# Kernel tuning notes

Hardware: AMD Instinct MI355X
Metric: run time of the kernel (lower is better)

The kernel has to match this reference:

```python
import jax, jax.numpy as jnp
import numpy as np

B, L, E, H = 2, 2048, 1024, 16
D = E // H


def setup_inputs() -> dict:
    key = jax.random.key(0)
    ks = jax.random.split(key, 6)
    s = 1.0 / np.sqrt(E)
    return {
        "X": jax.random.normal(ks[0], (B, L, E), dtype=jnp.float32),
        "ke_bias": jax.random.normal(ks[1], (B * H, L, L), dtype=jnp.float32) * 0.05,
        "in_proj_w": jax.random.normal(ks[2], (3 * E, E), dtype=jnp.float32) * s,
        "in_proj_b": jnp.zeros((3 * E,), dtype=jnp.float32),
        "out_proj_w": jax.random.normal(ks[3], (E, E), dtype=jnp.float32) * s,
        "out_proj_b": jnp.zeros((E,), dtype=jnp.float32),
    }


def reference(X, ke_bias, in_proj_w, in_proj_b, out_proj_w, out_proj_b):
    # Packed QKV projection, matching nn.MultiheadAttention layout.
    qkv = X @ in_proj_w.T + in_proj_b  # [B, L, 3E]
    q, k, v = jnp.split(qkv, 3, axis=-1)
    # [B, L, E] -> [B, H, L, D]
    q = q.reshape(B, L, H, D).transpose(0, 2, 1, 3)
    k = k.reshape(B, L, H, D).transpose(0, 2, 1, 3)
    v = v.reshape(B, L, H, D).transpose(0, 2, 1, 3)
    scale = 1.0 / jnp.sqrt(jnp.asarray(D, dtype=q.dtype))
    scores = jnp.einsum("bhqd,bhkd->bhqk", q * scale, k)
    scores = scores + ke_bias.reshape(B, H, L, L)  # additive knowledge bias
    A = jax.nn.softmax(scores, axis=-1)
    ctx = jnp.einsum("bhqk,bhkd->bhqd", A, v)  # [B, H, L, D]
    ctx = ctx.transpose(0, 2, 1, 3).reshape(B, L, E)
    return ctx @ out_proj_w.T + out_proj_b
```

## Files before the change

### kernel.cpp

```cpp
#include <hip/hip_runtime.h>
#include <stdint.h>

typedef __attribute__((ext_vector_type(4))) float f32x4;
typedef __attribute__((ext_vector_type(8))) short bf16x8;
typedef __attribute__((ext_vector_type(4))) short bf16x4;

#define MFMA(a, b, c) __builtin_amdgcn_mfma_f32_16x16x32_bf16(a, b, c, 0, 0, 0)

__device__ __forceinline__ short f2bf(float f) {
    unsigned u = __builtin_bit_cast(unsigned, f);
    u = (u + 0x7fffu + ((u >> 16) & 1u)) >> 16;
    return (short)u;
}

__device__ __forceinline__ void g2l16(const void* g, void* l) {
    __builtin_amdgcn_global_load_lds(
        (const __attribute__((address_space(1))) unsigned*)g,
        (__attribute__((address_space(3))) unsigned*)l, 16, 0, 0);
}

__global__ void cvt_bf16_kernel(const float* __restrict__ src,
                                short* __restrict__ dst, int n8) {
    int i = blockIdx.x * blockDim.x + threadIdx.x;
    if (i >= n8) return;
    const f32x4* s = (const f32x4*)src;
    f32x4 a = s[2 * i], b = s[2 * i + 1];
    bf16x8 o;
    o[0] = f2bf(a[0]); o[1] = f2bf(a[1]); o[2] = f2bf(a[2]); o[3] = f2bf(a[3]);
    o[4] = f2bf(b[0]); o[5] = f2bf(b[1]); o[6] = f2bf(b[2]); o[7] = f2bf(b[3]);
    ((bf16x8*)dst)[i] = o;
}

__global__ __launch_bounds__(256, 2) void gemm_qkv_kernel(
    const short* __restrict__ A, const short* __restrict__ W,
    const float* __restrict__ bias,
    short* __restrict__ qb, short* __restrict__ kb, short* __restrict__ vtb) {
    __shared__ short As[128 * 32];
    __shared__ short Bs[128 * 32];
    __shared__ short scrS[4][16 * 24];
    const int tid = threadIdx.x;
    const int wave = tid >> 6, lane = tid & 63;
    const int al = lane >> 4, ac = lane & 15;
    const int m0 = blockIdx.x * 128;
    const int n0 = blockIdx.y * 128;
    const int wm = wave & 1, wn = wave >> 1;

    const int crow = tid >> 2, ccol = (tid & 3) * 8;
    const short* Ag0 = A + (m0 + crow) * 1024 + ccol;
    const short* Ag1 = A + (m0 + crow + 64) * 1024 + ccol;
    const short* Wg0 = W + (n0 + crow) * 1024 + ccol;
    const short* Wg1 = W + (n0 + crow + 64) * 1024 + ccol;
    short* lA0 = &As[wave * 512];
    short* lA1 = &As[2048 + wave * 512];
    short* lB0 = &Bs[wave * 512];
    short* lB1 = &Bs[2048 + wave * 512];

    f32x4 acc[4][4];
#pragma unroll
    for (int mi = 0; mi < 4; mi++)
#pragma unroll
        for (int ni = 0; ni < 4; ni++) acc[mi][ni] = (f32x4){0.f, 0.f, 0.f, 0.f};

    for (int k0 = 0; k0 < 1024; k0 += 32) {
        __syncthreads();
        g2l16(Ag0 + k0, lA0);
        g2l16(Ag1 + k0, lA1);
        g2l16(Wg0 + k0, lB0);
        g2l16(Wg1 + k0, lB1);
        __syncthreads();
        bf16x8 af[4], bfr[4];
#pragma unroll
        for (int i = 0; i < 4; i++) {
            af[i] = *(const bf16x8*)&As[(wm * 64 + i * 16 + ac) * 32 + al * 8];
            bfr[i] = *(const bf16x8*)&Bs[(wn * 64 + i * 16 + ac) * 32 + al * 8];
        }
#pragma unroll
        for (int mi = 0; mi < 4; mi++)
#pragma unroll
            for (int ni = 0; ni < 4; ni++)
                acc[mi][ni] = MFMA(af[mi], bfr[ni], acc[mi][ni]);
    }

    const int n0w = n0 + wn * 64;
    const int which = n0w >> 10;
    short* scr = scrS[wave];
    const int lr = lane >> 2;
    const int lq = lane & 3;
    const int bglob = m0 >> 11;

#pragma unroll
    for (int mi = 0; mi < 4; mi++) {
#pragma unroll
        for (int ni = 0; ni < 4; ni++) {
            const int col0 = n0w + ni * 16;
            const float bvc = bias[col0 + ac];
            if (which == 2) {
                bf16x4 pk;
#pragma unroll
                for (int r = 0; r < 4; r++) pk[r] = f2bf(acc[mi][ni][r] + bvc);
                *(bf16x4*)&scr[ac * 24 + al * 4] = pk;
                bf16x4 v4 = *(const bf16x4*)&scr[lr * 24 + lq * 4];
                const int colv = col0 + lr;
                const int e = colv & 1023;
                const int h = e >> 6, d = e & 63;
                const int row0 = m0 + wm * 64 + mi * 16 + lq * 4;
                const int l0 = row0 & 2047;
                *(bf16x4*)&vtb[(((bglob * 16 + h) * 64 + d) * 2048) + l0] = v4;
            } else {
                const float sc = (which == 0) ? 0.125f : 1.0f;
#pragma unroll
                for (int r = 0; r < 4; r++)
                    scr[(al * 4 + r) * 24 + ac] = f2bf((acc[mi][ni][r] + bvc) * sc);
                bf16x4 v4 = *(const bf16x4*)&scr[lr * 24 + lq * 4];
                const int col = col0 + lq * 4;
                const int e = col & 1023;
                const int h = e >> 6, d0 = e & 63;
                const int row = m0 + wm * 64 + mi * 16 + lr;
                const int l = row & 2047;
                short* dst = (which == 0) ? qb : kb;
                *(bf16x4*)&dst[(((bglob * 16 + h) * 2048 + l) * 64) + d0] = v4;
            }
        }
    }
}

__global__ __launch_bounds__(256, 4) void attn_kernel(
    const short* __restrict__ Qb, const short* __restrict__ Kb,
    const short* __restrict__ Vtb, const float* __restrict__ bias,
    short* __restrict__ Ctx) {
    __shared__ short Qs[64 * 72];
    __shared__ short Ks[64 * 72];
    __shared__ short Vs[64 * 72];
    __shared__ short Ps[4][16 * 72];
    const int tid = threadIdx.x;
    const int wave = tid >> 6, lane = tid & 63;
    const int al = lane >> 4, ac = lane & 15;
    const int q0 = blockIdx.x * 64;
    const int bh = blockIdx.y;
    const long long kvbase = (long long)bh * (2048 * 64);

    const int sr = tid >> 3, sg = (tid & 7) * 8;

    *(bf16x8*)&Qs[sr * 72 + sg] = *(const bf16x8*)&Qb[kvbase + (q0 + sr) * 64 + sg];
    *(bf16x8*)&Qs[(sr + 32) * 72 + sg] =
        *(const bf16x8*)&Qb[kvbase + (q0 + sr + 32) * 64 + sg];
    __syncthreads();
    const bf16x8 qf0 = *(const bf16x8*)&Qs[(wave * 16 + ac) * 72 + al * 8];
    const bf16x8 qf1 = *(const bf16x8*)&Qs[(wave * 16 + ac) * 72 + al * 8 + 32];

    float m_i[4], l_i[4];
    f32x4 o[4];
#pragma unroll
    for (int r = 0; r < 4; r++) { m_i[r] = -1e30f; l_i[r] = 0.f; }
#pragma unroll
    for (int ni = 0; ni < 4; ni++) o[ni] = (f32x4){0.f, 0.f, 0.f, 0.f};

    const float L2E = 1.44269504088896340736f;
    const float* bp =
        bias + ((long long)bh * 2048 + q0 + wave * 16 + al * 4) * 2048 + ac;

    bf16x8 kr0 = *(const bf16x8*)&Kb[kvbase + sr * 64 + sg];
    bf16x8 kr1 = *(const bf16x8*)&Kb[kvbase + (sr + 32) * 64 + sg];
    bf16x8 vr0 = *(const bf16x8*)&Vtb[kvbase + sr * 2048 + sg];
    bf16x8 vr1 = *(const bf16x8*)&Vtb[kvbase + (sr + 32) * 2048 + sg];
    float bc[16];
#pragma unroll
    for (int ni = 0; ni < 4; ni++)
#pragma unroll
        for (int r = 0; r < 4; r++) bc[ni * 4 + r] = bp[r * 2048 + ni * 16];

#pragma unroll 2
    for (int kbk = 0; kbk < 32; ++kbk) {
        __syncthreads();
        *(bf16x8*)&Ks[sr * 72 + sg] = kr0;
        *(bf16x8*)&Ks[(sr + 32) * 72 + sg] = kr1;
        *(bf16x8*)&Vs[sr * 72 + sg] = vr0;
        *(bf16x8*)&Vs[(sr + 32) * 72 + sg] = vr1;
        __syncthreads();

        const int k1 = (kbk + 1) * 64;
        if (kbk < 31) {
            kr0 = *(const bf16x8*)&Kb[kvbase + (k1 + sr) * 64 + sg];
            kr1 = *(const bf16x8*)&Kb[kvbase + (k1 + sr + 32) * 64 + sg];
            vr0 = *(const bf16x8*)&Vtb[kvbase + sr * 2048 + k1 + sg];
            vr1 = *(const bf16x8*)&Vtb[kvbase + (sr + 32) * 2048 + k1 + sg];
        }

        f32x4 s[4];
#pragma unroll
        for (int ni = 0; ni < 4; ni++) {
            const bf16x8 kf0 = *(const bf16x8*)&Ks[(ni * 16 + ac) * 72 + al * 8];
            const bf16x8 kf1 =
                *(const bf16x8*)&Ks[(ni * 16 + ac) * 72 + al * 8 + 32];
            s[ni] = MFMA(qf0, kf0, ((f32x4){0.f, 0.f, 0.f, 0.f}));
            s[ni] = MFMA(qf1, kf1, s[ni]);
        }
        float mloc[4] = {-1e30f, -1e30f, -1e30f, -1e30f};
#pragma unroll
        for (int ni = 0; ni < 4; ni++)
#pragma unroll
            for (int r = 0; r < 4; r++) {
                float v = (s[ni][r] + bc[ni * 4 + r]) * L2E;
                s[ni][r] = v;
                mloc[r] = fmaxf(mloc[r], v);
            }
#pragma unroll
        for (int r = 0; r < 4; r++) {
#pragma unroll
            for (int off = 1; off < 16; off <<= 1)
                mloc[r] = fmaxf(mloc[r], __shfl_xor(mloc[r], off));
            const float mn = fmaxf(m_i[r], mloc[r]);
            const float a = __builtin_exp2f(m_i[r] - mn);
            m_i[r] = mn;
            l_i[r] *= a;
#pragma unroll
            for (int ni = 0; ni < 4; ni++) o[ni][r] *= a;
        }
        float rs[4] = {0.f, 0.f, 0.f, 0.f};
#pragma unroll
        for (int ni = 0; ni < 4; ni++)
#pragma unroll
            for (int r = 0; r < 4; r++) {
                const float p = __builtin_exp2f(s[ni][r] - m_i[r]);
                rs[r] += p;
                Ps[wave][(al * 4 + r) * 72 + ni * 16 + ac] = f2bf(p);
            }
#pragma unroll
        for (int r = 0; r < 4; r++) {
#pragma unroll
            for (int off = 1; off < 16; off <<= 1) rs[r] += __shfl_xor(rs[r], off);
            l_i[r] += rs[r];
        }

        float bn[16];
        if (kbk < 31) {
#pragma unroll
            for (int ni = 0; ni < 4; ni++)
#pragma unroll
                for (int r = 0; r < 4; r++)
                    bn[ni * 4 + r] = bp[r * 2048 + k1 + ni * 16];
        }

        const bf16x8 pf0 = *(const bf16x8*)&Ps[wave][ac * 72 + al * 8];
        const bf16x8 pf1 = *(const bf16x8*)&Ps[wave][ac * 72 + al * 8 + 32];
#pragma unroll
        for (int ni = 0; ni < 4; ni++) {
            const bf16x8 vf0 = *(const bf16x8*)&Vs[(ni * 16 + ac) * 72 + al * 8];
            const bf16x8 vf1 =
                *(const bf16x8*)&Vs[(ni * 16 + ac) * 72 + al * 8 + 32];
            o[ni] = MFMA(pf0, vf0, o[ni]);
            o[ni] = MFMA(pf1, vf1, o[ni]);
        }
#pragma unroll
        for (int i = 0; i < 16; i++) bc[i] = bn[i];
    }

    const int b = bh >> 4, h = bh & 15;
#pragma unroll
    for (int r = 0; r < 4; r++) {
        const float inv = 1.f / l_i[r];
        const int qrow = q0 + wave * 16 + al * 4 + r;
#pragma unroll
        for (int ni = 0; ni < 4; ni++) {
            const int d = ni * 16 + ac;
            Ctx[((long long)(b * 2048 + qrow)) * 1024 + h * 64 + d] =
                f2bf(o[ni][r] * inv);
        }
    }
}

__global__ __launch_bounds__(256, 2) void gemm_out_kernel(
    const short* __restrict__ A, const short* __restrict__ W,
    const float* __restrict__ bias, float* __restrict__ out) {
    __shared__ short As[128 * 32];
    __shared__ short Bs[128 * 32];
    __shared__ float scrF[4][16 * 28];
    const int tid = threadIdx.x;
    const int wave = tid >> 6, lane = tid & 63;
    const int al = lane >> 4, ac = lane & 15;
    const int m0 = blockIdx.x * 128;
    const int n0 = blockIdx.y * 128;
    const int wm = wave & 1, wn = wave >> 1;

    const int crow = tid >> 2, ccol = (tid & 3) * 8;
    const short* Ag0 = A + (m0 + crow) * 1024 + ccol;
    const short* Ag1 = A + (m0 + crow + 64) * 1024 + ccol;
    const short* Wg0 = W + (n0 + crow) * 1024 + ccol;
    const short* Wg1 = W + (n0 + crow + 64) * 1024 + ccol;
    short* lA0 = &As[wave * 512];
    short* lA1 = &As[2048 + wave * 512];
    short* lB0 = &Bs[wave * 512];
    short* lB1 = &Bs[2048 + wave * 512];

    f32x4 acc[4][4];
#pragma unroll
    for (int mi = 0; mi < 4; mi++)
#pragma unroll
        for (int ni = 0; ni < 4; ni++) acc[mi][ni] = (f32x4){0.f, 0.f, 0.f, 0.f};

    for (int k0 = 0; k0 < 1024; k0 += 32) {
        __syncthreads();
        g2l16(Ag0 + k0, lA0);
        g2l16(Ag1 + k0, lA1);
        g2l16(Wg0 + k0, lB0);
        g2l16(Wg1 + k0, lB1);
        __syncthreads();
        bf16x8 af[4], bfr[4];
#pragma unroll
        for (int i = 0; i < 4; i++) {
            af[i] = *(const bf16x8*)&As[(wm * 64 + i * 16 + ac) * 32 + al * 8];
            bfr[i] = *(const bf16x8*)&Bs[(wn * 64 + i * 16 + ac) * 32 + al * 8];
        }
#pragma unroll
        for (int mi = 0; mi < 4; mi++)
#pragma unroll
            for (int ni = 0; ni < 4; ni++)
                acc[mi][ni] = MFMA(af[mi], bfr[ni], acc[mi][ni]);
    }

    float* scr = scrF[wave];
    const int lr = lane >> 2, lq = lane & 3;
#pragma unroll
    for (int mi = 0; mi < 4; mi++) {
#pragma unroll
        for (int ni = 0; ni < 4; ni++) {
            const int col0 = n0 + wn * 64 + ni * 16;
            const float bvc = bias[col0 + ac];
#pragma unroll
            for (int r = 0; r < 4; r++)
                scr[(al * 4 + r) * 28 + ac] = acc[mi][ni][r] + bvc;
            f32x4 v4 = *(const f32x4*)&scr[lr * 28 + lq * 4];
            const int row = m0 + wm * 64 + mi * 16 + lr;
            *(f32x4*)&out[row * 1024 + col0 + lq * 4] = v4;
        }
    }
}

extern "C" void kernel_launch(void* const* d_in, const int* in_sizes, int n_in,
                              void* d_out, int out_size, void* d_ws,
                              size_t ws_size, hipStream_t stream) {
    const float* X = (const float*)d_in[0];
    const float* keb = (const float*)d_in[1];
    const float* Wi = (const float*)d_in[2];
    const float* bi = (const float*)d_in[3];
    const float* Wo = (const float*)d_in[4];
    const float* bo = (const float*)d_in[5];
    float* out = (float*)d_out;

    char* ws = (char*)d_ws;
    short* Xb  = (short*)(ws);
    short* Wib = (short*)(ws + 8388608);
    short* Wob = (short*)(ws + 14680064);
    short* Qb  = (short*)(ws + 16777216);
    short* Kb  = (short*)(ws + 25165824);
    short* Vtb = (short*)(ws + 33554432);
    short* Ctx = (short*)(ws + 41943040);

    cvt_bf16_kernel<<<dim3(524288 / 256), 256, 0, stream>>>(X, Xb, 524288);
    cvt_bf16_kernel<<<dim3(393216 / 256), 256, 0, stream>>>(Wi, Wib, 393216);
    cvt_bf16_kernel<<<dim3(131072 / 256), 256, 0, stream>>>(Wo, Wob, 131072);
    gemm_qkv_kernel<<<dim3(32, 24), 256, 0, stream>>>(Xb, Wib, bi, Qb, Kb, Vtb);
    attn_kernel<<<dim3(32, 32), 256, 0, stream>>>(Qb, Kb, Vtb, keb, Ctx);
    gemm_out_kernel<<<dim3(32, 8), 256, 0, stream>>>(Ctx, Wob, bo, out);
}
```

Before: 799.7 us.

## Rewrite attention as single-wave LDS-free kernel with transposed S and lazy rescale

The attention kernel becomes one-wave blocks over 16 query rows. K and V fragments are read straight from global memory into registers, so the LDS staging and block barriers are gone. S is computed transposed so the bias can be loaded as float4 nontemporal vectors, and log2e is folded into the Q scale and a bias FMA. Packed bf16 conversion builds the P fragment in registers, rescaling of the output is skipped unless the max grows by more than 8, and setprio is placed around the MFMAs. The risks are more redundant global/L2 traffic for K and V across blocks and a changed block-to-head mapping.

```diff
diff --git a/kernel.cpp b/kernel.cpp
--- a/kernel.cpp
+++ b/kernel.cpp
@@ -13,11 +13,20 @@
     return (short)u;
 }
 
+__device__ __forceinline__ unsigned cvt_pk_bf16(float lo, float hi) {
+    unsigned r;
+    asm("v_cvt_pk_bf16_f32 %0, %1, %2" : "=v"(r) : "v"(lo), "v"(hi));
+    return r;
+}
+
 __device__ __forceinline__ void g2l16(const void* g, void* l) {
     __builtin_amdgcn_global_load_lds(
         (const __attribute__((address_space(1))) unsigned*)g,
         (__attribute__((address_space(3))) unsigned*)l, 16, 0, 0);
 }
+
+union U8 { bf16x8 v; unsigned u[4]; };
+union V8 { bf16x8 v; bf16x4 h[2]; };
 
 __global__ void cvt_bf16_kernel(const float* __restrict__ src,
                                 short* __restrict__ dst, int n8) {
@@ -107,7 +116,7 @@
                 const int l0 = row0 & 2047;
                 *(bf16x4*)&vtb[(((bglob * 16 + h) * 64 + d) * 2048) + l0] = v4;
             } else {
-                const float sc = (which == 0) ? 0.125f : 1.0f;
+                const float sc = (which == 0) ? 0.18033688f : 1.0f;
 #pragma unroll
                 for (int r = 0; r < 4; r++)
                     scr[(al * 4 + r) * 24 + ac] = f2bf((acc[mi][ni][r] + bvc) * sc);
@@ -124,148 +133,129 @@
     }
 }
 
-__global__ __launch_bounds__(256, 4) void attn_kernel(
+#define ATTN_STEP(K0, BC, BN)                                                 \
+  {                                                                           \
+    const int kp_ = ((K0) + 64 < 2048) ? (K0) + 64 : 1984;                    \
+    f32x4 s_[4];                                                              \
+    __builtin_amdgcn_s_setprio(1);                                            \
+    _Pragma("unroll") for (int ni = 0; ni < 4; ni++) {                        \
+        s_[ni] = MFMA(kf[2 * ni], qf0, ((f32x4){0.f, 0.f, 0.f, 0.f}));        \
+        s_[ni] = MFMA(kf[2 * ni + 1], qf1, s_[ni]);                           \
+    }                                                                         \
+    __builtin_amdgcn_s_setprio(0);                                            \
+             \
+    _Pragma("unroll") for (int ni = 0; ni < 4; ni++) {                        \
+        kf[2 * ni] = *(const bf16x8*)&kpb[(kp_ + ni * 16) * 64];              \
+        kf[2 * ni + 1] = *(const bf16x8*)&kpb[(kp_ + ni * 16) * 64 + 32];     \
+    }                                                                         \
+        \
+    V8 vf_[4][2];                                                             \
+    _Pragma("unroll") for (int nd = 0; nd < 4; nd++)                          \
+        _Pragma("unroll") for (int ss = 0; ss < 2; ss++) {                    \
+            const short* vp_ = vpb + nd * (16 * 2048) + (K0) + 32 * ss;       \
+            vf_[nd][ss].h[0] = *(const bf16x4*)vp_;                           \
+            vf_[nd][ss].h[1] = *(const bf16x4*)(vp_ + 16);                    \
+        }                                                                     \
+         \
+    _Pragma("unroll") for (int ni = 0; ni < 4; ni++)                          \
+        BN[ni] = __builtin_nontemporal_load((const f32x4*)&bp[kp_ + ni * 16]);\
+    float t_[16];                                                             \
+    _Pragma("unroll") for (int ni = 0; ni < 4; ni++)                          \
+        _Pragma("unroll") for (int r = 0; r < 4; r++)                         \
+            t_[ni * 4 + r] = __builtin_fmaf(BC[ni][r], L2E, s_[ni][r]);       \
+    float ma_[8];                                                             \
+    _Pragma("unroll") for (int i = 0; i < 8; i++)                             \
+        ma_[i] = fmaxf(t_[i], t_[8 + i]);                                     \
+    float ml_ = fmaxf(fmaxf(fmaxf(ma_[0], ma_[1]), fmaxf(ma_[2], ma_[3])),    \
+                      fmaxf(fmaxf(ma_[4], ma_[5]), fmaxf(ma_[6], ma_[7])));   \
+    ml_ = fmaxf(ml_, __shfl_xor(ml_, 16));                                    \
+    ml_ = fmaxf(ml_, __shfl_xor(ml_, 32));                                    \
+    if (__any(ml_ > m_i + 8.f)) {                \
+        const float mn_ = fmaxf(m_i, ml_);                                    \
+        const float a_ = __builtin_exp2f(m_i - mn_);                          \
+        m_i = mn_;                                                            \
+        l_i *= a_;                                                            \
+        _Pragma("unroll") for (int r = 0; r < 4; r++) {                       \
+            const float ar_ = __shfl(a_, al20 + r);                           \
+            _Pragma("unroll") for (int nd = 0; nd < 4; nd++)                  \
+                o[nd][r] *= ar_;                                              \
+        }                                                                     \
+    }                                                                         \
+    float p_[16];                                                             \
+    _Pragma("unroll") for (int i = 0; i < 16; i++)                            \
+        p_[i] = __builtin_exp2f(t_[i] - m_i);                                 \
+    float ps0_ = 0.f, ps1_ = 0.f, ps2_ = 0.f, ps3_ = 0.f;                     \
+    _Pragma("unroll") for (int r = 0; r < 4; r++) {                           \
+        ps0_ += p_[r]; ps1_ += p_[4 + r];                                     \
+        ps2_ += p_[8 + r]; ps3_ += p_[12 + r];                                \
+    }                                                                         \
+    l_i += (ps0_ + ps1_) + (ps2_ + ps3_);                                     \
+    U8 pf0_, pf1_;                                                            \
+    _Pragma("unroll") for (int w = 0; w < 4; w++) {                           \
+        pf0_.u[w] = cvt_pk_bf16(p_[2 * w], p_[2 * w + 1]);                    \
+        pf1_.u[w] = cvt_pk_bf16(p_[8 + 2 * w], p_[8 + 2 * w + 1]);            \
+    }                                                                         \
+    __builtin_amdgcn_s_setprio(1);                                            \
+    _Pragma("unroll") for (int nd = 0; nd < 4; nd++) {                        \
+        o[nd] = MFMA(pf0_.v, vf_[nd][0].v, o[nd]);                            \
+        o[nd] = MFMA(pf1_.v, vf_[nd][1].v, o[nd]);                            \
+    }                                                                         \
+    __builtin_amdgcn_s_setprio(0);                                            \
+  }
+
+__global__ __launch_bounds__(64, 3) void attn_kernel(
     const short* __restrict__ Qb, const short* __restrict__ Kb,
     const short* __restrict__ Vtb, const float* __restrict__ bias,
     short* __restrict__ Ctx) {
-    __shared__ short Qs[64 * 72];
-    __shared__ short Ks[64 * 72];
-    __shared__ short Vs[64 * 72];
-    __shared__ short Ps[4][16 * 72];
-    const int tid = threadIdx.x;
-    const int wave = tid >> 6, lane = tid & 63;
-    const int al = lane >> 4, ac = lane & 15;
-    const int q0 = blockIdx.x * 64;
-    const int bh = blockIdx.y;
+    const int lane = threadIdx.x & 63;
+    const int ac = lane & 15, al = lane >> 4;
+    const int al20 = al * 20;
+    const int bid = blockIdx.x;
+    const int bh = (bid & 7) * 4 + ((bid >> 3) >> 7);
+    const int q0 = ((bid >> 3) & 127) * 16;
     const long long kvbase = (long long)bh * (2048 * 64);
-
-    const int sr = tid >> 3, sg = (tid & 7) * 8;
-
-    *(bf16x8*)&Qs[sr * 72 + sg] = *(const bf16x8*)&Qb[kvbase + (q0 + sr) * 64 + sg];
-    *(bf16x8*)&Qs[(sr + 32) * 72 + sg] =
-        *(const bf16x8*)&Qb[kvbase + (q0 + sr + 32) * 64 + sg];
-    __syncthreads();
-    const bf16x8 qf0 = *(const bf16x8*)&Qs[(wave * 16 + ac) * 72 + al * 8];
-    const bf16x8 qf1 = *(const bf16x8*)&Qs[(wave * 16 + ac) * 72 + al * 8 + 32];
-
-    float m_i[4], l_i[4];
+    const float L2E = 1.44269504088896340736f;
+
+    const short* qp = Qb + kvbase + (q0 + ac) * 64 + al * 8;
+    const bf16x8 qf0 = *(const bf16x8*)qp;
+    const bf16x8 qf1 = *(const bf16x8*)(qp + 32);
+    const float* bp = bias + ((long long)bh * 2048 + q0 + ac) * 2048 + al * 4;
+    const short* kpb = Kb + kvbase + ac * 64 + al * 8;
+    const short* vpb = Vtb + kvbase + ac * 2048 + al * 4;
+
+    float m_i = -1e30f, l_i = 0.f;
     f32x4 o[4];
 #pragma unroll
-    for (int r = 0; r < 4; r++) { m_i[r] = -1e30f; l_i[r] = 0.f; }
-#pragma unroll
-    for (int ni = 0; ni < 4; ni++) o[ni] = (f32x4){0.f, 0.f, 0.f, 0.f};
-
-    const float L2E = 1.44269504088896340736f;
-    const float* bp =
-        bias + ((long long)bh * 2048 + q0 + wave * 16 + al * 4) * 2048 + ac;
-
-    bf16x8 kr0 = *(const bf16x8*)&Kb[kvbase + sr * 64 + sg];
-    bf16x8 kr1 = *(const bf16x8*)&Kb[kvbase + (sr + 32) * 64 + sg];
-    bf16x8 vr0 = *(const bf16x8*)&Vtb[kvbase + sr * 2048 + sg];
-    bf16x8 vr1 = *(const bf16x8*)&Vtb[kvbase + (sr + 32) * 2048 + sg];
-    float bc[16];
+    for (int i = 0; i < 4; i++) o[i] = (f32x4){0.f, 0.f, 0.f, 0.f};
+
+    bf16x8 kf[8];
+#pragma unroll
+    for (int ni = 0; ni < 4; ni++) {
+        kf[2 * ni] = *(const bf16x8*)&kpb[(ni * 16) * 64];
+        kf[2 * ni + 1] = *(const bf16x8*)&kpb[(ni * 16) * 64 + 32];
+    }
+    f32x4 bcA[4], bcB[4];
 #pragma unroll
     for (int ni = 0; ni < 4; ni++)
-#pragma unroll
-        for (int r = 0; r < 4; r++) bc[ni * 4 + r] = bp[r * 2048 + ni * 16];
-
-#pragma unroll 2
-    for (int kbk = 0; kbk < 32; ++kbk) {
-        __syncthreads();
-        *(bf16x8*)&Ks[sr * 72 + sg] = kr0;
-        *(bf16x8*)&Ks[(sr + 32) * 72 + sg] = kr1;
-        *(bf16x8*)&Vs[sr * 72 + sg] = vr0;
-        *(bf16x8*)&Vs[(sr + 32) * 72 + sg] = vr1;
-        __syncthreads();
-
-        const int k1 = (kbk + 1) * 64;
-        if (kbk < 31) {
-            kr0 = *(const bf16x8*)&Kb[kvbase + (k1 + sr) * 64 + sg];
-            kr1 = *(const bf16x8*)&Kb[kvbase + (k1 + sr + 32) * 64 + sg];
-            vr0 = *(const bf16x8*)&Vtb[kvbase + sr * 2048 + k1 + sg];
-            vr1 = *(const bf16x8*)&Vtb[kvbase + (sr + 32) * 2048 + k1 + sg];
-        }
-
-        f32x4 s[4];
-#pragma unroll
-        for (int ni = 0; ni < 4; ni++) {
-            const bf16x8 kf0 = *(const bf16x8*)&Ks[(ni * 16 + ac) * 72 + al * 8];
-            const bf16x8 kf1 =
-                *(const bf16x8*)&Ks[(ni * 16 + ac) * 72 + al * 8 + 32];
-            s[ni] = MFMA(qf0, kf0, ((f32x4){0.f, 0.f, 0.f, 0.f}));
-            s[ni] = MFMA(qf1, kf1, s[ni]);
-        }
-        float mloc[4] = {-1e30f, -1e30f, -1e30f, -1e30f};
-#pragma unroll
-        for (int ni = 0; ni < 4; ni++)
-#pragma unroll
-            for (int r = 0; r < 4; r++) {
-                float v = (s[ni][r] + bc[ni * 4 + r]) * L2E;
-                s[ni][r] = v;
-                mloc[r] = fmaxf(mloc[r], v);
-            }
-#pragma unroll
-        for (int r = 0; r < 4; r++) {
-#pragma unroll
-            for (int off = 1; off < 16; off <<= 1)
-                mloc[r] = fmaxf(mloc[r], __shfl_xor(mloc[r], off));
-            const float mn = fmaxf(m_i[r], mloc[r]);
-            const float a = __builtin_exp2f(m_i[r] - mn);
-            m_i[r] = mn;
-            l_i[r] *= a;
-#pragma unroll
-            for (int ni = 0; ni < 4; ni++) o[ni][r] *= a;
-        }
-        float rs[4] = {0.f, 0.f, 0.f, 0.f};
-#pragma unroll
-        for (int ni = 0; ni < 4; ni++)
-#pragma unroll
-            for (int r = 0; r < 4; r++) {
-                const float p = __builtin_exp2f(s[ni][r] - m_i[r]);
-                rs[r] += p;
-                Ps[wave][(al * 4 + r) * 72 + ni * 16 + ac] = f2bf(p);
-            }
-#pragma unroll
-        for (int r = 0; r < 4; r++) {
-#pragma unroll
-            for (int off = 1; off < 16; off <<= 1) rs[r] += __shfl_xor(rs[r], off);
-            l_i[r] += rs[r];
-        }
-
-        float bn[16];
-        if (kbk < 31) {
-#pragma unroll
-            for (int ni = 0; ni < 4; ni++)
-#pragma unroll
-                for (int r = 0; r < 4; r++)
-                    bn[ni * 4 + r] = bp[r * 2048 + k1 + ni * 16];
-        }
-
-        const bf16x8 pf0 = *(const bf16x8*)&Ps[wave][ac * 72 + al * 8];
-        const bf16x8 pf1 = *(const bf16x8*)&Ps[wave][ac * 72 + al * 8 + 32];
-#pragma unroll
-        for (int ni = 0; ni < 4; ni++) {
-            const bf16x8 vf0 = *(const bf16x8*)&Vs[(ni * 16 + ac) * 72 + al * 8];
-            const bf16x8 vf1 =
-                *(const bf16x8*)&Vs[(ni * 16 + ac) * 72 + al * 8 + 32];
-            o[ni] = MFMA(pf0, vf0, o[ni]);
-            o[ni] = MFMA(pf1, vf1, o[ni]);
-        }
-#pragma unroll
-        for (int i = 0; i < 16; i++) bc[i] = bn[i];
-    }
-
-    const int b = bh >> 4, h = bh & 15;
+        bcA[ni] = __builtin_nontemporal_load((const f32x4*)&bp[ni * 16]);
+
+    for (int k0 = 0; k0 < 2048; k0 += 128) {
+        ATTN_STEP(k0, bcA, bcB);
+        ATTN_STEP(k0 + 64, bcB, bcA);
+    }
+
+    float lt = l_i + __shfl_xor(l_i, 16);
+    lt += __shfl_xor(lt, 32);
+    const float inv = 1.f / lt;
+    const int b_ = bh >> 4, h_ = bh & 15;
+    short* cp = Ctx + (long long)(b_ * 2048 + q0) * 1024 + h_ * 64 + ac;
 #pragma unroll
     for (int r = 0; r < 4; r++) {
-        const float inv = 1.f / l_i[r];
-        const int qrow = q0 + wave * 16 + al * 4 + r;
-#pragma unroll
-        for (int ni = 0; ni < 4; ni++) {
-            const int d = ni * 16 + ac;
-            Ctx[((long long)(b * 2048 + qrow)) * 1024 + h * 64 + d] =
-                f2bf(o[ni][r] * inv);
-        }
+        const float ir_ = __shfl(inv, al20 + r);
+        const int row = al * 4 + r;
+#pragma unroll
+        for (int nd = 0; nd < 4; nd++)
+            cp[(long long)row * 1024 + nd * 16] = f2bf(o[nd][r] * ir_);
     }
 }
 
@@ -360,6 +350,6 @@
     cvt_bf16_kernel<<<dim3(393216 / 256), 256, 0, stream>>>(Wi, Wib, 393216);
     cvt_bf16_kernel<<<dim3(131072 / 256), 256, 0, stream>>>(Wo, Wob, 131072);
     gemm_qkv_kernel<<<dim3(32, 24), 256, 0, stream>>>(Xb, Wib, bi, Qb, Kb, Vtb);
-    attn_kernel<<<dim3(32, 32), 256, 0, stream>>>(Qb, Kb, Vtb, keb, Ctx);
+    attn_kernel<<<dim3(4096), 64, 0, stream>>>(Qb, Kb, Vtb, keb, Ctx);
     gemm_out_kernel<<<dim3(32, 8), 256, 0, stream>>>(Ctx, Wob, bo, out);
 }
```

New measurement: 1.050 ms. 1.31x slower.
